# Kernel optimization log

Hardware: AMD Instinct MI355X
Metric: run time of the kernel (lower is better)

## Reference

```python
import jax, jax.numpy as jnp
import numpy as np

N = 20000      # total nodes (20 proteins x 1000 residues)
E = 320000     # edges (avg degree 16)
F_IN = 22      # amino-acid feature dim
H = 4          # attention heads
C = 64         # hidden dim per head
HC = H * C     # 256
G = 20         # number of graphs
OUT = 128      # output embedding dim
NEG_SLOPE = 0.2


def setup_inputs() -> dict:
    key = jax.random.key(0)
    ks = jax.random.split(key, 24)
    x = jax.random.normal(ks[0], (N, F_IN), dtype=jnp.float32)
    edge_index = jax.random.randint(ks[1], (2, E), 0, N)
    batch = jnp.arange(N, dtype=jnp.int64) // (N // G)  # 1000 nodes per graph
    s = 0.1
    d = {
        'x': x, 'edge_index': edge_index, 'batch': batch,
        'Win': jax.random.normal(ks[2], (F_IN, C)) * s,
        'bin_': jnp.zeros((C,), jnp.float32),
        'Wout': jax.random.normal(ks[3], (2 * HC, OUT)) * s,
        'bout': jnp.zeros((OUT,), jnp.float32),
    }
    kidx = 4
    for i in range(3):
        in_dim = C if i == 0 else HC
        d[f'Wl{i}'] = jax.random.normal(ks[kidx], (in_dim, HC)) * s; kidx += 1
        d[f'Wr{i}'] = jax.random.normal(ks[kidx], (in_dim, HC)) * s; kidx += 1
        d[f'att{i}'] = jax.random.normal(ks[kidx], (H, C)) * s; kidx += 1
        d[f'b{i}'] = jnp.zeros((HC,), jnp.float32)
    return d


def _gatv2_layer(h, src, dst, Wl, Wr, att, bias):
    # PyG GATv2Conv (share_weights=False, concat=True), dropout off (eval)
    xl = (h @ Wl).reshape(-1, H, C)   # source transform (x_j)
    xr = (h @ Wr).reshape(-1, H, C)   # target transform (x_i)
    e = jax.nn.leaky_relu(xl[src] + xr[dst], NEG_SLOPE)  # [E+N, H, C]
    logit = jnp.einsum('ehc,hc->eh', e, att)             # [E+N, H]
    mx = jax.ops.segment_max(logit, dst, num_segments=N)
    mx = jnp.where(jnp.isfinite(mx), mx, 0.0)
    ex = jnp.exp(logit - mx[dst])
    den = jax.ops.segment_sum(ex, dst, num_segments=N)
    alpha = ex / (den[dst] + 1e-16)                      # segment softmax
    out = jax.ops.segment_sum(alpha[:, :, None] * xl[src], dst, num_segments=N)
    return out.reshape(-1, HC) + bias


def reference(x, edge_index, batch, Win, bin_,
              Wl0, Wr0, att0, b0, Wl1, Wr1, att1, b1, Wl2, Wr2, att2, b2,
              Wout, bout):
    # add self-loops once (add_self_loops=True in every GATv2Conv)
    loops = jnp.arange(N, dtype=edge_index.dtype)
    src = jnp.concatenate([edge_index[0], loops])
    dst = jnp.concatenate([edge_index[1], loops])

    h = jax.nn.relu(x @ Win + bin_)  # input_proj + ReLU (dropout = eval identity)
    layers = [(Wl0, Wr0, att0, b0), (Wl1, Wr1, att1, b1), (Wl2, Wr2, att2, b2)]
    for (Wl, Wr, att, b) in layers:
        h_prev = h
        h = jax.nn.elu(_gatv2_layer(h, src, dst, Wl, Wr, att, b))
        if h_prev.shape[-1] == h.shape[-1]:  # residual when dims match (layers 1,2)
            h = h + h_prev

    counts = jax.ops.segment_sum(jnp.ones((N,), h.dtype), batch, num_segments=G)
    x_mean = jax.ops.segment_sum(h, batch, num_segments=G) / counts[:, None]
    x_max = jax.ops.segment_max(h, batch, num_segments=G)
    x_global = jnp.concatenate([x_mean, x_max], axis=-1)  # [G, 512]
    return x_global @ Wout + bout                          # [G, 128]
```

## Files before the change

kernel.cpp:

```cpp
#include <hip/hip_runtime.h>
#include <hip/hip_bf16.h>
#include <math.h>

#define N_NODES 20000
#define N_EDGES 320000
#define F_IN 22
#define H_HEADS 4
#define C_DIM 64
#define HC 256
#define G_GRAPHS 20
#define OUT_DIM 128
#define NODES_PER_G 1000
#define POOL_CHUNKS 8
#define NODES_PER_CHUNK (NODES_PER_G / POOL_CHUNKS)
#define ELL_CAP 64
#define SCAT_NB ((N_EDGES + 255) / 256)
#define INPROJ_NB (N_NODES / 4)
#define GAT_NB (N_NODES / 4)
#define GAT_CPX (GAT_NB / 8)

#if __has_builtin(__builtin_amdgcn_exp2f)
#define EXP2F __builtin_amdgcn_exp2f
#else
#define EXP2F exp2f
#endif

typedef unsigned short ushortT;
typedef __attribute__((ext_vector_type(8))) short short8;
typedef __attribute__((ext_vector_type(4))) float v4f;
typedef __attribute__((ext_vector_type(2))) float f2;

typedef const __attribute__((address_space(1))) void* gas_p;
typedef __attribute__((address_space(3))) void* las_p;

__device__ inline ushortT f2bf(float f) {
    unsigned int u = __float_as_uint(f);
    unsigned int r = (u + 0x7fffu + ((u >> 16) & 1u)) >> 16;
    return (ushortT)r;
}

__global__ __launch_bounds__(256) void front_kernel(
        const int* __restrict__ esrc, const int* __restrict__ edst,
        int* __restrict__ fill, int* __restrict__ ell,
        const float* __restrict__ x, const float* __restrict__ Win,
        const float* __restrict__ bin, ushortT* __restrict__ h0b,
        const float* __restrict__ Wl0, const float* __restrict__ Wr0,
        const float* __restrict__ Wl1, const float* __restrict__ Wr1,
        const float* __restrict__ Wl2, const float* __restrict__ Wr2,
        ushortT* __restrict__ Bt0, ushortT* __restrict__ Bt1, ushortT* __restrict__ Bt2) {
    int tid = threadIdx.x;
    if (blockIdx.x < SCAT_NB) {
        int i = blockIdx.x * 256 + tid;
        if (i < N_EDGES) {
            int d = edst[i];
            int p = atomicAdd(&fill[d], 1);
            if (p < ELL_CAP) ell[(d << 6) + p] = esrc[i];
        }
        return;
    }
    if (blockIdx.x < SCAT_NB + INPROJ_NB) {
        int node = (blockIdx.x - SCAT_NB) * 4 + (tid >> 6);
        int c = tid & 63;
        float acc = bin[c];
        const float* xr = x + node * F_IN;
#pragma unroll
        for (int f = 0; f < F_IN; f++) acc += xr[f] * Win[f * C_DIM + c];
        h0b[node * C_DIM + c] = f2bf(acc > 0.f ? acc : 0.f);
        return;
    }
    int flat = blockIdx.x - SCAT_NB - INPROJ_NB;
    int z = flat >> 6;
    int rem = flat & 63;
    int kx = (rem >> 3) * 32;
    int nx = (rem & 7) * 32;
    int layer = z >> 1, isR = z & 1;
    const float* src; ushortT* dst; int K;
    if (layer == 0)      { K = 64;  dst = Bt0; src = isR ? Wr0 : Wl0; }
    else if (layer == 1) { K = 256; dst = Bt1; src = isR ? Wr1 : Wl1; }
    else                 { K = 256; dst = Bt2; src = isR ? Wr2 : Wl2; }
    if (kx >= K) return;
    __shared__ float tile[32][33];
    int c = tid & 31, r8 = tid >> 5;
#pragma unroll
    for (int i = 0; i < 4; i++) {
        int kk = r8 + i * 8;
        tile[kk][c] = src[(kx + kk) * 256 + nx + c];
    }
    __syncthreads();
    int nbase = isR ? 256 : 0;
#pragma unroll
    for (int i = 0; i < 4; i++) {
        int nn = r8 + i * 8;
        dst[(size_t)(nbase + nx + nn) * K + kx + c] = f2bf(tile[c][nn]);
    }
}

#define GBM 128
#define GBN 128
#define GBK 32

__global__ __launch_bounds__(256) void gemm_mfma_kernel(
        const ushortT* __restrict__ A, const ushortT* __restrict__ Bt,
        ushortT* __restrict__ XLb, ushortT* __restrict__ XRb, int M, int K) {
    __shared__ ushortT As[GBM * GBK];
    __shared__ ushortT Bs[GBN * GBK];
    int tid = threadIdx.x;
    int wave = tid >> 6, lane = tid & 63;
    int wm = wave & 1, wn = wave >> 1;
    int bm0 = blockIdx.y * GBM;
    int bn0 = blockIdx.x * GBN;

    v4f acc[4][4];
#pragma unroll
    for (int mt = 0; mt < 4; mt++)
#pragma unroll
        for (int nt = 0; nt < 4; nt++) acc[mt][nt] = (v4f){0.f, 0.f, 0.f, 0.f};

    int srow = lane >> 2;
    int scol = (lane & 3) * 8;
    int arow0 = wave * 16 + srow;
    int arow1 = arow0 + 64;
    int ag0 = bm0 + arow0; if (ag0 >= M) ag0 = 0;
    int ag1 = bm0 + arow1; if (ag1 >= M) ag1 = 0;
    const ushortT* aptr0 = A + (size_t)ag0 * K + scol;
    const ushortT* aptr1 = A + (size_t)ag1 * K + scol;
    const ushortT* bptr0 = Bt + (size_t)(bn0 + arow0) * K + scol;
    const ushortT* bptr1 = Bt + (size_t)(bn0 + arow1) * K + scol;
    las_p lA0 = (las_p)&As[(wave * 16) * GBK];
    las_p lA1 = (las_p)&As[(wave * 16 + 64) * GBK];
    las_p lB0 = (las_p)&Bs[(wave * 16) * GBK];
    las_p lB1 = (las_p)&Bs[(wave * 16 + 64) * GBK];

    int mrow = lane & 15;
    int koff = (lane >> 4) * 8;

    for (int k0 = 0; k0 < K; k0 += GBK) {
        __builtin_amdgcn_global_load_lds((gas_p)(aptr0 + k0), lA0, 16, 0, 0);
        __builtin_amdgcn_global_load_lds((gas_p)(aptr1 + k0), lA1, 16, 0, 0);
        __builtin_amdgcn_global_load_lds((gas_p)(bptr0 + k0), lB0, 16, 0, 0);
        __builtin_amdgcn_global_load_lds((gas_p)(bptr1 + k0), lB1, 16, 0, 0);
        __syncthreads();
        short8 af[4], bf[4];
#pragma unroll
        for (int mt = 0; mt < 4; mt++)
            af[mt] = *(const short8*)&As[(wm * 64 + mt * 16 + mrow) * GBK + koff];
#pragma unroll
        for (int nt = 0; nt < 4; nt++)
            bf[nt] = *(const short8*)&Bs[(wn * 64 + nt * 16 + mrow) * GBK + koff];
#pragma unroll
        for (int mt = 0; mt < 4; mt++)
#pragma unroll
            for (int nt = 0; nt < 4; nt++)
                acc[mt][nt] = __builtin_amdgcn_mfma_f32_16x16x32_bf16(af[mt], bf[nt], acc[mt][nt], 0, 0, 0);
        __syncthreads();
    }

    int cbase = bn0 + wn * 64;
    ushortT* dst = XLb;
    if (cbase >= 256) { dst = XRb; cbase -= 256; }
    int col = cbase + (lane & 15);
    int rbase = bm0 + wm * 64 + ((lane >> 4) * 4);
#pragma unroll
    for (int mt = 0; mt < 4; mt++) {
#pragma unroll
        for (int reg = 0; reg < 4; reg++) {
            int row = rbase + mt * 16 + reg;
            if (row < M) {
#pragma unroll
                for (int nt = 0; nt < 4; nt++)
                    dst[(size_t)row * 256 + col + nt * 16] = f2bf(acc[mt][nt][reg]);
            }
        }
    }
}

template <int PAT>
__device__ inline float swz_add(float p) {
    return p + __int_as_float(__builtin_amdgcn_ds_swizzle(__float_as_int(p), PAT));
}

__device__ inline void gat_edge(uint2 curu, f2 xr01, f2 xr23, f2 at01, f2 at23,
                                float live, float& den, f2& acc01, f2& acc23) {
    f2 x01, x23;
    x01.x = __uint_as_float(curu.x << 16);
    x01.y = __uint_as_float(curu.x & 0xffff0000u);
    x23.x = __uint_as_float(curu.y << 16);
    x23.y = __uint_as_float(curu.y & 0xffff0000u);
    f2 t01 = x01 + xr01;
    f2 t23 = x23 + xr23;
    t01 = __builtin_elementwise_max(t01, t01 * 0.2f);
    t23 = __builtin_elementwise_max(t23, t23 * 0.2f);
    f2 pp = t01 * at01;
    pp = __builtin_elementwise_fma(t23, at23, pp);
    float p = pp.x + pp.y;
    p = swz_add<0x041F>(p);
    p = swz_add<0x081F>(p);
    p = swz_add<0x101F>(p);
    p = swz_add<0x201F>(p);
    p = fminf(p, 110.f);
    float w = EXP2F(p) * live;
    den += w;
    f2 wv = {w, w};
    acc01 = __builtin_elementwise_fma(wv, x01, acc01);
    acc23 = __builtin_elementwise_fma(wv, x23, acc23);
}

__global__ __launch_bounds__(256) void gat_layer_kernel(
        const ushortT* __restrict__ xlb, const ushortT* __restrict__ xrb,
        const int* __restrict__ ell, const int* __restrict__ fill,
        const float* __restrict__ att, const float* __restrict__ bias,
        const float* __restrict__ hprev,
        float* __restrict__ hout, ushortT* __restrict__ houtb) {
    int lane = threadIdx.x & 63;
    int bid = blockIdx.x;
    int lb = (bid & 7) * GAT_CPX + (bid >> 3);
    int d = lb * 4 + (threadIdx.x >> 6);

    const uint2* xl2 = (const uint2*)xlb;
    uint2 xru = ((const uint2*)xrb)[d * 64 + lane];
    f2 xr01, xr23;
    xr01.x = __uint_as_float(xru.x << 16);
    xr01.y = __uint_as_float(xru.x & 0xffff0000u);
    xr23.x = __uint_as_float(xru.y << 16);
    xr23.y = __uint_as_float(xru.y & 0xffff0000u);

    float4 attv = ((const float4*)att)[lane];
    const float LOG2E = 1.44269504088896f;
    f2 at01 = {attv.x * LOG2E, attv.y * LOG2E};
    f2 at23 = {attv.z * LOG2E, attv.w * LOG2E};

    int deg = fill[d];
    if (deg > ELL_CAP - 1) deg = ELL_CAP - 1;
    int M = deg + 1;

    int idx = (lane < deg) ? ell[(d << 6) + lane] : d;

    float den = 0.f;
    f2 acc01 = {0.f, 0.f}, acc23 = {0.f, 0.f};

    uint2 buf[4];
#pragma unroll
    for (int k = 0; k < 4; k++) {
        int ni = __builtin_amdgcn_readlane(idx, k);
        buf[k] = xl2[(size_t)ni * 64 + lane];
    }
    int P = (M + 3) >> 2;
    for (int g = 0; g < P; g++) {
        int base = g * 4;
#pragma unroll
        for (int k = 0; k < 4; k++) {
            uint2 cur = buf[k];
            int ni = __builtin_amdgcn_readlane(idx, (base + 4 + k) & 63);
            buf[k] = xl2[(size_t)ni * 64 + lane];
            float live = (base + k < M) ? 1.0f : 0.0f;
            gat_edge(cur, xr01, xr23, at01, at23, live, den, acc01, acc23);
        }
    }

    float inv = 1.f / (den + 1e-16f);
    float4 bv = ((const float4*)bias)[lane];
    float4 v;
    v.x = acc01.x * inv + bv.x;
    v.y = acc01.y * inv + bv.y;
    v.z = acc23.x * inv + bv.z;
    v.w = acc23.y * inv + bv.w;
    v.x = v.x > 0.f ? v.x : __expf(v.x) - 1.f;
    v.y = v.y > 0.f ? v.y : __expf(v.y) - 1.f;
    v.z = v.z > 0.f ? v.z : __expf(v.z) - 1.f;
    v.w = v.w > 0.f ? v.w : __expf(v.w) - 1.f;
    if (hprev) {
        float4 hp = ((const float4*)hprev)[d * 64 + lane];
        v.x += hp.x; v.y += hp.y; v.z += hp.z; v.w += hp.w;
    }
    if (hout) ((float4*)hout)[d * 64 + lane] = v;
    uint2 pb;
    pb.x = (unsigned int)f2bf(v.x) | ((unsigned int)f2bf(v.y) << 16);
    pb.y = (unsigned int)f2bf(v.z) | ((unsigned int)f2bf(v.w) << 16);
    ((uint2*)houtb)[d * 64 + lane] = pb;
}

__global__ __launch_bounds__(256) void pool_partial_kernel(
        const ushortT* __restrict__ hb, float* __restrict__ psum, float* __restrict__ pmax) {
    int blk = blockIdx.x;
    int tid = threadIdx.x;
    int g = blk / POOL_CHUNKS;
    int ch = blk % POOL_CHUNKS;
    const ushortT* base = hb + ((size_t)g * NODES_PER_G + ch * NODES_PER_CHUNK) * HC;
    float sum = 0.f, mx = -INFINITY;
    for (int n = 0; n < NODES_PER_CHUNK; n++) {
        float v = __uint_as_float(((unsigned int)base[n * HC + tid]) << 16);
        sum += v;
        mx = fmaxf(mx, v);
    }
    psum[blk * HC + tid] = sum;
    pmax[blk * HC + tid] = mx;
}

__global__ __launch_bounds__(256) void pool_out_kernel(
        const float* __restrict__ psum, const float* __restrict__ pmax,
        const float* __restrict__ Wout, const float* __restrict__ bout,
        float* __restrict__ out) {
    int g = blockIdx.x;
    int tid = threadIdx.x;
    __shared__ float xg[2 * HC];
    float sum = 0.f, mx = -INFINITY;
    for (int c = 0; c < POOL_CHUNKS; c++) {
        sum += psum[(g * POOL_CHUNKS + c) * HC + tid];
        mx = fmaxf(mx, pmax[(g * POOL_CHUNKS + c) * HC + tid]);
    }
    xg[tid] = sum * (1.0f / NODES_PER_G);
    xg[HC + tid] = mx;
    __syncthreads();
    if (tid < OUT_DIM) {
        float acc = bout[tid];
        for (int j = 0; j < 2 * HC; j++) acc += xg[j] * Wout[j * OUT_DIM + tid];
        out[g * OUT_DIM + tid] = acc;
    }
}


extern "C" void kernel_launch(void* const* d_in, const int* in_sizes, int n_in,
                              void* d_out, int out_size, void* d_ws, size_t ws_size,
                              hipStream_t stream) {
    const float* x    = (const float*)d_in[0];
    const int*   ei   = (const int*)d_in[1];
    const float* Win  = (const float*)d_in[3];
    const float* bin  = (const float*)d_in[4];
    const float* Wout = (const float*)d_in[5];
    const float* bout = (const float*)d_in[6];
    const float* Wl[3] = {(const float*)d_in[7],  (const float*)d_in[11], (const float*)d_in[15]};
    const float* Wr[3] = {(const float*)d_in[8],  (const float*)d_in[12], (const float*)d_in[16]};
    const float* att[3] = {(const float*)d_in[9], (const float*)d_in[13], (const float*)d_in[17]};
    const float* bb[3] = {(const float*)d_in[10], (const float*)d_in[14], (const float*)d_in[18]};
    float* out = (float*)d_out;

    const int* esrc = ei;
    const int* edst = ei + N_EDGES;

    float* hA   = (float*)d_ws;
    float* hB   = hA + (size_t)N_NODES * HC;
    float* psum = hB + (size_t)N_NODES * HC;
    float* pmax = psum + (size_t)G_GRAPHS * POOL_CHUNKS * HC;
    ushortT* h0b = (ushortT*)(pmax + (size_t)G_GRAPHS * POOL_CHUNKS * HC);
    ushortT* hAb = h0b + (size_t)N_NODES * C_DIM;
    ushortT* hBb = hAb + (size_t)N_NODES * HC;
    ushortT* XLb = hBb + (size_t)N_NODES * HC;
    ushortT* XRb = XLb + (size_t)N_NODES * HC;
    ushortT* Bt0 = XRb + (size_t)N_NODES * HC;
    ushortT* Bt1 = Bt0 + 512 * 64;
    ushortT* Bt2 = Bt1 + 512 * 256;
    int* fill  = (int*)(Bt2 + 512 * 256);
    int* ell   = fill + N_NODES;

    (void)hipMemsetAsync(fill, 0, N_NODES * sizeof(int), stream);

    front_kernel<<<SCAT_NB + INPROJ_NB + 384, 256, 0, stream>>>(
        esrc, edst, fill, ell, x, Win, bin, h0b,
        Wl[0], Wr[0], Wl[1], Wr[1], Wl[2], Wr[2], Bt0, Bt1, Bt2);

    dim3 ggrid(512 / GBN, (N_NODES + GBM - 1) / GBM);

    gemm_mfma_kernel<<<ggrid, 256, 0, stream>>>(h0b, Bt0, XLb, XRb, N_NODES, C_DIM);
    gat_layer_kernel<<<GAT_NB, 256, 0, stream>>>(XLb, XRb, ell, fill, att[0], bb[0],
                                                 nullptr, hA, hAb);

    gemm_mfma_kernel<<<ggrid, 256, 0, stream>>>(hAb, Bt1, XLb, XRb, N_NODES, HC);
    gat_layer_kernel<<<GAT_NB, 256, 0, stream>>>(XLb, XRb, ell, fill, att[1], bb[1],
                                                 hA, hB, hBb);

    gemm_mfma_kernel<<<ggrid, 256, 0, stream>>>(hBb, Bt2, XLb, XRb, N_NODES, HC);
    gat_layer_kernel<<<GAT_NB, 256, 0, stream>>>(XLb, XRb, ell, fill, att[2], bb[2],
                                                 hB, nullptr, hAb);

    pool_partial_kernel<<<G_GRAPHS * POOL_CHUNKS, 256, 0, stream>>>(hAb, psum, pmax);
    pool_out_kernel<<<G_GRAPHS, 256, 0, stream>>>(psum, pmax, Wout, bout, out);
}
```

Baseline: 263.1 us.

## Process two edges per wavefront with 16-byte loads per lane in GAT layer

Splits each 64-lane wavefront into two 32-lane halves. Each half handles a different neighbor edge and each lane loads 8 bf16 features as a uint4 instead of 4. The head-dot reduction drops one swizzle step, and the halves' partial softmax sums and accumulators are combined with a cross-half shuffle at the end. This aims to halve loop iterations and widen the gather loads, at the cost of more registers, a final reduction, and idle lanes in the store phase.

Measured after the change: 263.3 us. Within noise of the previous version (+0.1%).

```diff
diff --git a/kernel.cpp b/kernel.cpp
--- a/kernel.cpp
+++ b/kernel.cpp
@@ -179,30 +179,44 @@
     return p + __int_as_float(__builtin_amdgcn_ds_swizzle(__float_as_int(p), PAT));
 }
 
-__device__ inline void gat_edge(uint2 curu, f2 xr01, f2 xr23, f2 at01, f2 at23,
-                                float live, float& den, f2& acc01, f2& acc23) {
-    f2 x01, x23;
+__device__ inline void gat_edge2(uint4 curu,
+        f2 xr01, f2 xr23, f2 xr45, f2 xr67,
+        f2 a01, f2 a23, f2 a45, f2 a67,
+        float live, float& den,
+        f2& acc01, f2& acc23, f2& acc45, f2& acc67) {
+    f2 x01, x23, x45, x67;
     x01.x = __uint_as_float(curu.x << 16);
     x01.y = __uint_as_float(curu.x & 0xffff0000u);
     x23.x = __uint_as_float(curu.y << 16);
     x23.y = __uint_as_float(curu.y & 0xffff0000u);
+    x45.x = __uint_as_float(curu.z << 16);
+    x45.y = __uint_as_float(curu.z & 0xffff0000u);
+    x67.x = __uint_as_float(curu.w << 16);
+    x67.y = __uint_as_float(curu.w & 0xffff0000u);
     f2 t01 = x01 + xr01;
     f2 t23 = x23 + xr23;
+    f2 t45 = x45 + xr45;
+    f2 t67 = x67 + xr67;
     t01 = __builtin_elementwise_max(t01, t01 * 0.2f);
     t23 = __builtin_elementwise_max(t23, t23 * 0.2f);
-    f2 pp = t01 * at01;
-    pp = __builtin_elementwise_fma(t23, at23, pp);
+    t45 = __builtin_elementwise_max(t45, t45 * 0.2f);
+    t67 = __builtin_elementwise_max(t67, t67 * 0.2f);
+    f2 pp = t01 * a01;
+    pp = __builtin_elementwise_fma(t23, a23, pp);
+    pp = __builtin_elementwise_fma(t45, a45, pp);
+    pp = __builtin_elementwise_fma(t67, a67, pp);
     float p = pp.x + pp.y;
     p = swz_add<0x041F>(p);
     p = swz_add<0x081F>(p);
     p = swz_add<0x101F>(p);
-    p = swz_add<0x201F>(p);
     p = fminf(p, 110.f);
     float w = EXP2F(p) * live;
     den += w;
     f2 wv = {w, w};
     acc01 = __builtin_elementwise_fma(wv, x01, acc01);
     acc23 = __builtin_elementwise_fma(wv, x23, acc23);
+    acc45 = __builtin_elementwise_fma(wv, x45, acc45);
+    acc67 = __builtin_elementwise_fma(wv, x67, acc67);
 }
 
 __global__ __launch_bounds__(256) void gat_layer_kernel(
@@ -212,22 +226,32 @@
         const float* __restrict__ hprev,
         float* __restrict__ hout, ushortT* __restrict__ houtb) {
     int lane = threadIdx.x & 63;
+    int q = lane & 31;
+    int half = lane >> 5;
     int bid = blockIdx.x;
     int lb = (bid & 7) * GAT_CPX + (bid >> 3);
     int d = lb * 4 + (threadIdx.x >> 6);
 
-    const uint2* xl2 = (const uint2*)xlb;
-    uint2 xru = ((const uint2*)xrb)[d * 64 + lane];
-    f2 xr01, xr23;
+    const uint4* xl4 = (const uint4*)xlb;
+    uint4 xru = ((const uint4*)xrb)[d * 32 + q];
+    f2 xr01, xr23, xr45, xr67;
     xr01.x = __uint_as_float(xru.x << 16);
     xr01.y = __uint_as_float(xru.x & 0xffff0000u);
     xr23.x = __uint_as_float(xru.y << 16);
     xr23.y = __uint_as_float(xru.y & 0xffff0000u);
-
-    float4 attv = ((const float4*)att)[lane];
+    xr45.x = __uint_as_float(xru.z << 16);
+    xr45.y = __uint_as_float(xru.z & 0xffff0000u);
+    xr67.x = __uint_as_float(xru.w << 16);
+    xr67.y = __uint_as_float(xru.w & 0xffff0000u);
+
+    const float4* att4 = (const float4*)att;
+    float4 av0 = att4[q * 2];
+    float4 av1 = att4[q * 2 + 1];
     const float LOG2E = 1.44269504088896f;
-    f2 at01 = {attv.x * LOG2E, attv.y * LOG2E};
-    f2 at23 = {attv.z * LOG2E, attv.w * LOG2E};
+    f2 a01 = {av0.x * LOG2E, av0.y * LOG2E};
+    f2 a23 = {av0.z * LOG2E, av0.w * LOG2E};
+    f2 a45 = {av1.x * LOG2E, av1.y * LOG2E};
+    f2 a67 = {av1.z * LOG2E, av1.w * LOG2E};
 
     int deg = fill[d];
     if (deg > ELL_CAP - 1) deg = ELL_CAP - 1;
@@ -236,47 +260,81 @@
     int idx = (lane < deg) ? ell[(d << 6) + lane] : d;
 
     float den = 0.f;
-    f2 acc01 = {0.f, 0.f}, acc23 = {0.f, 0.f};
-
-    uint2 buf[4];
-#pragma unroll
-    for (int k = 0; k < 4; k++) {
-        int ni = __builtin_amdgcn_readlane(idx, k);
-        buf[k] = xl2[(size_t)ni * 64 + lane];
-    }
-    int P = (M + 3) >> 2;
-    for (int g = 0; g < P; g++) {
-        int base = g * 4;
-#pragma unroll
-        for (int k = 0; k < 4; k++) {
-            uint2 cur = buf[k];
-            int ni = __builtin_amdgcn_readlane(idx, (base + 4 + k) & 63);
-            buf[k] = xl2[(size_t)ni * 64 + lane];
-            float live = (base + k < M) ? 1.0f : 0.0f;
-            gat_edge(cur, xr01, xr23, at01, at23, live, den, acc01, acc23);
+    f2 acc01 = {0.f, 0.f}, acc23 = {0.f, 0.f}, acc45 = {0.f, 0.f}, acc67 = {0.f, 0.f};
+
+    uint4 buf[2];
+#pragma unroll
+    for (int k = 0; k < 2; k++) {
+        int sA = __builtin_amdgcn_readlane(idx, 2 * k);
+        int sB = __builtin_amdgcn_readlane(idx, 2 * k + 1);
+        int ni = half ? sB : sA;
+        buf[k] = xl4[(size_t)ni * 32 + q];
+    }
+    int P2 = (M + 1) >> 1;
+    int G = (P2 + 1) >> 1;
+    for (int g = 0; g < G; g++) {
+#pragma unroll
+        for (int k = 0; k < 2; k++) {
+            uint4 cur = buf[k];
+            int np = 2 * g + 2 + k;
+            int sA = __builtin_amdgcn_readlane(idx, (2 * np) & 63);
+            int sB = __builtin_amdgcn_readlane(idx, (2 * np + 1) & 63);
+            int ni = half ? sB : sA;
+            buf[k] = xl4[(size_t)ni * 32 + q];
+            int slot = (2 * g + k) * 2 + half;
+            float live = (slot < M) ? 1.0f : 0.0f;
+            gat_edge2(cur, xr01, xr23, xr45, xr67, a01, a23, a45, a67,
+                      live, den, acc01, acc23, acc45, acc67);
         }
     }
 
+    den     += __shfl_xor(den, 32);
+    acc01.x += __shfl_xor(acc01.x, 32);
+    acc01.y += __shfl_xor(acc01.y, 32);
+    acc23.x += __shfl_xor(acc23.x, 32);
+    acc23.y += __shfl_xor(acc23.y, 32);
+    acc45.x += __shfl_xor(acc45.x, 32);
+    acc45.y += __shfl_xor(acc45.y, 32);
+    acc67.x += __shfl_xor(acc67.x, 32);
+    acc67.y += __shfl_xor(acc67.y, 32);
+
     float inv = 1.f / (den + 1e-16f);
-    float4 bv = ((const float4*)bias)[lane];
-    float4 v;
-    v.x = acc01.x * inv + bv.x;
-    v.y = acc01.y * inv + bv.y;
-    v.z = acc23.x * inv + bv.z;
-    v.w = acc23.y * inv + bv.w;
-    v.x = v.x > 0.f ? v.x : __expf(v.x) - 1.f;
-    v.y = v.y > 0.f ? v.y : __expf(v.y) - 1.f;
-    v.z = v.z > 0.f ? v.z : __expf(v.z) - 1.f;
-    v.w = v.w > 0.f ? v.w : __expf(v.w) - 1.f;
+    float4 bv0 = ((const float4*)bias)[q * 2];
+    float4 bv1 = ((const float4*)bias)[q * 2 + 1];
+    float v0 = acc01.x * inv + bv0.x;
+    float v1 = acc01.y * inv + bv0.y;
+    float v2 = acc23.x * inv + bv0.z;
+    float v3 = acc23.y * inv + bv0.w;
+    float v4 = acc45.x * inv + bv1.x;
+    float v5 = acc45.y * inv + bv1.y;
+    float v6 = acc67.x * inv + bv1.z;
+    float v7 = acc67.y * inv + bv1.w;
+    v0 = v0 > 0.f ? v0 : __expf(v0) - 1.f;
+    v1 = v1 > 0.f ? v1 : __expf(v1) - 1.f;
+    v2 = v2 > 0.f ? v2 : __expf(v2) - 1.f;
+    v3 = v3 > 0.f ? v3 : __expf(v3) - 1.f;
+    v4 = v4 > 0.f ? v4 : __expf(v4) - 1.f;
+    v5 = v5 > 0.f ? v5 : __expf(v5) - 1.f;
+    v6 = v6 > 0.f ? v6 : __expf(v6) - 1.f;
+    v7 = v7 > 0.f ? v7 : __expf(v7) - 1.f;
     if (hprev) {
-        float4 hp = ((const float4*)hprev)[d * 64 + lane];
-        v.x += hp.x; v.y += hp.y; v.z += hp.z; v.w += hp.w;
-    }
-    if (hout) ((float4*)hout)[d * 64 + lane] = v;
-    uint2 pb;
-    pb.x = (unsigned int)f2bf(v.x) | ((unsigned int)f2bf(v.y) << 16);
-    pb.y = (unsigned int)f2bf(v.z) | ((unsigned int)f2bf(v.w) << 16);
-    ((uint2*)houtb)[d * 64 + lane] = pb;
+        float4 h0 = ((const float4*)hprev)[d * 64 + q * 2];
+        float4 h1 = ((const float4*)hprev)[d * 64 + q * 2 + 1];
+        v0 += h0.x; v1 += h0.y; v2 += h0.z; v3 += h0.w;
+        v4 += h1.x; v5 += h1.y; v6 += h1.z; v7 += h1.w;
+    }
+    if (half == 0) {
+        if (hout) {
+            ((float4*)hout)[d * 64 + q * 2]     = (float4){v0, v1, v2, v3};
+            ((float4*)hout)[d * 64 + q * 2 + 1] = (float4){v4, v5, v6, v7};
+        }
+        uint4 pb;
+        pb.x = (unsigned int)f2bf(v0) | ((unsigned int)f2bf(v1) << 16);
+        pb.y = (unsigned int)f2bf(v2) | ((unsigned int)f2bf(v3) << 16);
+        pb.z = (unsigned int)f2bf(v4) | ((unsigned int)f2bf(v5) << 16);
+        pb.w = (unsigned int)f2bf(v6) | ((unsigned int)f2bf(v7) << 16);
+        ((uint4*)houtb)[d * 32 + q] = pb;
+    }
 }
 
 __global__ __launch_bounds__(256) void pool_partial_kernel(
```

## Fuse all stages into one persistent cooperative kernel with grid syncs

Applied to the files above, without the earlier changes.

Replaces the sequence of separate kernel launches (front, three GEMM+GAT pairs, pooling) with a single cooperative persistent kernel that loops over work tiles and separates phases with grid-wide barriers. It also turns the weight-transpose tiles into plain grid-stride loops and raises the pooling chunk count. The aim is to remove the launch overhead and inter-kernel gaps. In exchange, occupancy is capped by the cooperative grid size, grid.sync adds its own cost, and the GAT phase loses its earlier block-to-node remapping. The weight transpose now uses uncoalesced strided reads.

Result: slower. 845.3 us (+221.2%).

```diff
diff --git a/kernel.cpp b/kernel.cpp
--- a/kernel.cpp
+++ b/kernel.cpp
@@ -1,6 +1,9 @@
 #include <hip/hip_runtime.h>
+#include <hip/hip_cooperative_groups.h>
 #include <hip/hip_bf16.h>
 #include <math.h>
+
+namespace cg = cooperative_groups;
 
 #define N_NODES 20000
 #define N_EDGES 320000
@@ -11,13 +14,10 @@
 #define G_GRAPHS 20
 #define OUT_DIM 128
 #define NODES_PER_G 1000
-#define POOL_CHUNKS 8
+#define POOL_CHUNKS 50
 #define NODES_PER_CHUNK (NODES_PER_G / POOL_CHUNKS)
 #define ELL_CAP 64
-#define SCAT_NB ((N_EDGES + 255) / 256)
-#define INPROJ_NB (N_NODES / 4)
 #define GAT_NB (N_NODES / 4)
-#define GAT_CPX (GAT_NB / 8)
 
 #if __has_builtin(__builtin_amdgcn_exp2f)
 #define EXP2F __builtin_amdgcn_exp2f
@@ -38,137 +38,88 @@
     unsigned int r = (u + 0x7fffu + ((u >> 16) & 1u)) >> 16;
     return (ushortT)r;
 }
-
-__global__ __launch_bounds__(256) void front_kernel(
-        const int* __restrict__ esrc, const int* __restrict__ edst,
-        int* __restrict__ fill, int* __restrict__ ell,
-        const float* __restrict__ x, const float* __restrict__ Win,
-        const float* __restrict__ bin, ushortT* __restrict__ h0b,
-        const float* __restrict__ Wl0, const float* __restrict__ Wr0,
-        const float* __restrict__ Wl1, const float* __restrict__ Wr1,
-        const float* __restrict__ Wl2, const float* __restrict__ Wr2,
-        ushortT* __restrict__ Bt0, ushortT* __restrict__ Bt1, ushortT* __restrict__ Bt2) {
-    int tid = threadIdx.x;
-    if (blockIdx.x < SCAT_NB) {
-        int i = blockIdx.x * 256 + tid;
-        if (i < N_EDGES) {
-            int d = edst[i];
-            int p = atomicAdd(&fill[d], 1);
-            if (p < ELL_CAP) ell[(d << 6) + p] = esrc[i];
-        }
-        return;
-    }
-    if (blockIdx.x < SCAT_NB + INPROJ_NB) {
-        int node = (blockIdx.x - SCAT_NB) * 4 + (tid >> 6);
-        int c = tid & 63;
-        float acc = bin[c];
-        const float* xr = x + node * F_IN;
-#pragma unroll
-        for (int f = 0; f < F_IN; f++) acc += xr[f] * Win[f * C_DIM + c];
-        h0b[node * C_DIM + c] = f2bf(acc > 0.f ? acc : 0.f);
-        return;
-    }
-    int flat = blockIdx.x - SCAT_NB - INPROJ_NB;
-    int z = flat >> 6;
-    int rem = flat & 63;
-    int kx = (rem >> 3) * 32;
-    int nx = (rem & 7) * 32;
-    int layer = z >> 1, isR = z & 1;
-    const float* src; ushortT* dst; int K;
-    if (layer == 0)      { K = 64;  dst = Bt0; src = isR ? Wr0 : Wl0; }
-    else if (layer == 1) { K = 256; dst = Bt1; src = isR ? Wr1 : Wl1; }
-    else                 { K = 256; dst = Bt2; src = isR ? Wr2 : Wl2; }
-    if (kx >= K) return;
-    __shared__ float tile[32][33];
-    int c = tid & 31, r8 = tid >> 5;
-#pragma unroll
-    for (int i = 0; i < 4; i++) {
-        int kk = r8 + i * 8;
-        tile[kk][c] = src[(kx + kk) * 256 + nx + c];
-    }
-    __syncthreads();
-    int nbase = isR ? 256 : 0;
-#pragma unroll
-    for (int i = 0; i < 4; i++) {
-        int nn = r8 + i * 8;
-        dst[(size_t)(nbase + nx + nn) * K + kx + c] = f2bf(tile[c][nn]);
-    }
+__device__ inline float bf2f(ushortT u) {
+    return __uint_as_float(((unsigned int)u) << 16);
 }
 
 #define GBM 128
 #define GBN 128
 #define GBK 32
 
-__global__ __launch_bounds__(256) void gemm_mfma_kernel(
-        const ushortT* __restrict__ A, const ushortT* __restrict__ Bt,
-        ushortT* __restrict__ XLb, ushortT* __restrict__ XRb, int M, int K) {
-    __shared__ ushortT As[GBM * GBK];
-    __shared__ ushortT Bs[GBN * GBK];
+__device__ inline void gemm_phase(const ushortT* __restrict__ A,
+                                  const ushortT* __restrict__ Bt,
+                                  ushortT* __restrict__ XLb, ushortT* __restrict__ XRb,
+                                  int K, ushortT* As, ushortT* Bs) {
+    const int M = N_NODES;
+    const int MT = (N_NODES + GBM - 1) / GBM;
     int tid = threadIdx.x;
     int wave = tid >> 6, lane = tid & 63;
     int wm = wave & 1, wn = wave >> 1;
-    int bm0 = blockIdx.y * GBM;
-    int bn0 = blockIdx.x * GBN;
-
-    v4f acc[4][4];
-#pragma unroll
-    for (int mt = 0; mt < 4; mt++)
-#pragma unroll
-        for (int nt = 0; nt < 4; nt++) acc[mt][nt] = (v4f){0.f, 0.f, 0.f, 0.f};
-
-    int srow = lane >> 2;
-    int scol = (lane & 3) * 8;
-    int arow0 = wave * 16 + srow;
-    int arow1 = arow0 + 64;
-    int ag0 = bm0 + arow0; if (ag0 >= M) ag0 = 0;
-    int ag1 = bm0 + arow1; if (ag1 >= M) ag1 = 0;
-    const ushortT* aptr0 = A + (size_t)ag0 * K + scol;
-    const ushortT* aptr1 = A + (size_t)ag1 * K + scol;
-    const ushortT* bptr0 = Bt + (size_t)(bn0 + arow0) * K + scol;
-    const ushortT* bptr1 = Bt + (size_t)(bn0 + arow1) * K + scol;
-    las_p lA0 = (las_p)&As[(wave * 16) * GBK];
-    las_p lA1 = (las_p)&As[(wave * 16 + 64) * GBK];
-    las_p lB0 = (las_p)&Bs[(wave * 16) * GBK];
-    las_p lB1 = (las_p)&Bs[(wave * 16 + 64) * GBK];
-
-    int mrow = lane & 15;
-    int koff = (lane >> 4) * 8;
-
-    for (int k0 = 0; k0 < K; k0 += GBK) {
-        __builtin_amdgcn_global_load_lds((gas_p)(aptr0 + k0), lA0, 16, 0, 0);
-        __builtin_amdgcn_global_load_lds((gas_p)(aptr1 + k0), lA1, 16, 0, 0);
-        __builtin_amdgcn_global_load_lds((gas_p)(bptr0 + k0), lB0, 16, 0, 0);
-        __builtin_amdgcn_global_load_lds((gas_p)(bptr1 + k0), lB1, 16, 0, 0);
-        __syncthreads();
-        short8 af[4], bf[4];
+
+    for (int t = blockIdx.x; t < MT * 4; t += gridDim.x) {
+        int bm0 = (t >> 2) * GBM;
+        int bn0 = (t & 3) * GBN;
+
+        v4f acc[4][4];
 #pragma unroll
         for (int mt = 0; mt < 4; mt++)
-            af[mt] = *(const short8*)&As[(wm * 64 + mt * 16 + mrow) * GBK + koff];
-#pragma unroll
-        for (int nt = 0; nt < 4; nt++)
-            bf[nt] = *(const short8*)&Bs[(wn * 64 + nt * 16 + mrow) * GBK + koff];
-#pragma unroll
-        for (int mt = 0; mt < 4; mt++)
+#pragma unroll
+            for (int nt = 0; nt < 4; nt++) acc[mt][nt] = (v4f){0.f, 0.f, 0.f, 0.f};
+
+        int srow = lane >> 2;
+        int scol = (lane & 3) * 8;
+        int arow0 = wave * 16 + srow;
+        int arow1 = arow0 + 64;
+        int ag0 = bm0 + arow0; if (ag0 >= M) ag0 = 0;
+        int ag1 = bm0 + arow1; if (ag1 >= M) ag1 = 0;
+        const ushortT* aptr0 = A + (size_t)ag0 * K + scol;
+        const ushortT* aptr1 = A + (size_t)ag1 * K + scol;
+        const ushortT* bptr0 = Bt + (size_t)(bn0 + arow0) * K + scol;
+        const ushortT* bptr1 = Bt + (size_t)(bn0 + arow1) * K + scol;
+        las_p lA0 = (las_p)&As[(wave * 16) * GBK];
+        las_p lA1 = (las_p)&As[(wave * 16 + 64) * GBK];
+        las_p lB0 = (las_p)&Bs[(wave * 16) * GBK];
+        las_p lB1 = (las_p)&Bs[(wave * 16 + 64) * GBK];
+
+        int mrow = lane & 15;
+        int koff = (lane >> 4) * 8;
+
+        for (int k0 = 0; k0 < K; k0 += GBK) {
+            __builtin_amdgcn_global_load_lds((gas_p)(aptr0 + k0), lA0, 16, 0, 0);
+            __builtin_amdgcn_global_load_lds((gas_p)(aptr1 + k0), lA1, 16, 0, 0);
+            __builtin_amdgcn_global_load_lds((gas_p)(bptr0 + k0), lB0, 16, 0, 0);
+            __builtin_amdgcn_global_load_lds((gas_p)(bptr1 + k0), lB1, 16, 0, 0);
+            __syncthreads();
+            short8 af[4], bf[4];
+#pragma unroll
+            for (int mt = 0; mt < 4; mt++)
+                af[mt] = *(const short8*)&As[(wm * 64 + mt * 16 + mrow) * GBK + koff];
 #pragma unroll
             for (int nt = 0; nt < 4; nt++)
-                acc[mt][nt] = __builtin_amdgcn_mfma_f32_16x16x32_bf16(af[mt], bf[nt], acc[mt][nt], 0, 0, 0);
-        __syncthreads();
-    }
-
-    int cbase = bn0 + wn * 64;
-    ushortT* dst = XLb;
-    if (cbase >= 256) { dst = XRb; cbase -= 256; }
-    int col = cbase + (lane & 15);
-    int rbase = bm0 + wm * 64 + ((lane >> 4) * 4);
-#pragma unroll
-    for (int mt = 0; mt < 4; mt++) {
-#pragma unroll
-        for (int reg = 0; reg < 4; reg++) {
-            int row = rbase + mt * 16 + reg;
-            if (row < M) {
+                bf[nt] = *(const short8*)&Bs[(wn * 64 + nt * 16 + mrow) * GBK + koff];
+#pragma unroll
+            for (int mt = 0; mt < 4; mt++)
 #pragma unroll
                 for (int nt = 0; nt < 4; nt++)
-                    dst[(size_t)row * 256 + col + nt * 16] = f2bf(acc[mt][nt][reg]);
+                    acc[mt][nt] = __builtin_amdgcn_mfma_f32_16x16x32_bf16(af[mt], bf[nt], acc[mt][nt], 0, 0, 0);
+            __syncthreads();
+        }
+
+        int cbase = bn0 + wn * 64;
+        ushortT* dst = XLb;
+        if (cbase >= 256) { dst = XRb; cbase -= 256; }
+        int col = cbase + (lane & 15);
+        int rbase = bm0 + wm * 64 + ((lane >> 4) * 4);
+#pragma unroll
+        for (int mt = 0; mt < 4; mt++) {
+#pragma unroll
+            for (int reg = 0; reg < 4; reg++) {
+                int row = rbase + mt * 16 + reg;
+                if (row < M) {
+#pragma unroll
+                    for (int nt = 0; nt < 4; nt++)
+                        dst[(size_t)row * 256 + col + nt * 16] = f2bf(acc[mt][nt][reg]);
+                }
             }
         }
     }
@@ -205,116 +156,178 @@
     acc23 = __builtin_elementwise_fma(wv, x23, acc23);
 }
 
-__global__ __launch_bounds__(256) void gat_layer_kernel(
-        const ushortT* __restrict__ xlb, const ushortT* __restrict__ xrb,
-        const int* __restrict__ ell, const int* __restrict__ fill,
-        const float* __restrict__ att, const float* __restrict__ bias,
-        const float* __restrict__ hprev,
-        float* __restrict__ hout, ushortT* __restrict__ houtb) {
+__device__ inline void gat_phase(const ushortT* __restrict__ xlb, const ushortT* __restrict__ xrb,
+                                 const int* __restrict__ ell, const int* __restrict__ fill,
+                                 const float* __restrict__ att, const float* __restrict__ bias,
+                                 const float* __restrict__ hprev,
+                                 float* __restrict__ hout, ushortT* __restrict__ houtb) {
     int lane = threadIdx.x & 63;
+    const uint2* xl2 = (const uint2*)xlb;
+
+    for (int lb = blockIdx.x; lb < GAT_NB; lb += gridDim.x) {
+        int d = lb * 4 + (threadIdx.x >> 6);
+
+        uint2 xru = ((const uint2*)xrb)[d * 64 + lane];
+        f2 xr01, xr23;
+        xr01.x = __uint_as_float(xru.x << 16);
+        xr01.y = __uint_as_float(xru.x & 0xffff0000u);
+        xr23.x = __uint_as_float(xru.y << 16);
+        xr23.y = __uint_as_float(xru.y & 0xffff0000u);
+
+        float4 attv = ((const float4*)att)[lane];
+        const float LOG2E = 1.44269504088896f;
+        f2 at01 = {attv.x * LOG2E, attv.y * LOG2E};
+        f2 at23 = {attv.z * LOG2E, attv.w * LOG2E};
+
+        int deg = fill[d];
+        if (deg > ELL_CAP - 1) deg = ELL_CAP - 1;
+        int M = deg + 1;
+
+        int idx = (lane < deg) ? ell[(d << 6) + lane] : d;
+
+        float den = 0.f;
+        f2 acc01 = {0.f, 0.f}, acc23 = {0.f, 0.f};
+
+        uint2 buf[4];
+#pragma unroll
+        for (int k = 0; k < 4; k++) {
+            int ni = __builtin_amdgcn_readlane(idx, k);
+            buf[k] = xl2[(size_t)ni * 64 + lane];
+        }
+        int P = (M + 3) >> 2;
+        for (int g = 0; g < P; g++) {
+            int base = g * 4;
+#pragma unroll
+            for (int k = 0; k < 4; k++) {
+                uint2 cur = buf[k];
+                int ni = __builtin_amdgcn_readlane(idx, (base + 4 + k) & 63);
+                buf[k] = xl2[(size_t)ni * 64 + lane];
+                float live = (base + k < M) ? 1.0f : 0.0f;
+                gat_edge(cur, xr01, xr23, at01, at23, live, den, acc01, acc23);
+            }
+        }
+
+        float inv = 1.f / (den + 1e-16f);
+        float4 bv = ((const float4*)bias)[lane];
+        float4 v;
+        v.x = acc01.x * inv + bv.x;
+        v.y = acc01.y * inv + bv.y;
+        v.z = acc23.x * inv + bv.z;
+        v.w = acc23.y * inv + bv.w;
+        v.x = v.x > 0.f ? v.x : __expf(v.x) - 1.f;
+        v.y = v.y > 0.f ? v.y : __expf(v.y) - 1.f;
+        v.z = v.z > 0.f ? v.z : __expf(v.z) - 1.f;
+        v.w = v.w > 0.f ? v.w : __expf(v.w) - 1.f;
+        if (hprev) {
+            float4 hp = ((const float4*)hprev)[d * 64 + lane];
+            v.x += hp.x; v.y += hp.y; v.z += hp.z; v.w += hp.w;
+        }
+        if (hout) ((float4*)hout)[d * 64 + lane] = v;
+        uint2 pb;
+        pb.x = (unsigned int)f2bf(v.x) | ((unsigned int)f2bf(v.y) << 16);
+        pb.y = (unsigned int)f2bf(v.z) | ((unsigned int)f2bf(v.w) << 16);
+        ((uint2*)houtb)[d * 64 + lane] = pb;
+    }
+}
+
+struct MegaParams {
+    const int *esrc, *edst;
+    int *fill, *ell;
+    const float *x, *Win, *bin;
+    ushortT *h0b;
+    const float *Wl0, *Wr0, *Wl1, *Wr1, *Wl2, *Wr2;
+    ushortT *Bt0, *Bt1, *Bt2;
+    ushortT *XLb, *XRb;
+    const float *att0, *b0, *att1, *b1, *att2, *b2;
+    float *hA, *hB;
+    ushortT *hAb, *hBb;
+    float *psum, *pmax;
+    const float *Wout, *bout;
+    float *out;
+};
+
+__global__ __launch_bounds__(256, 4) void mega_kernel(MegaParams p) {
+    cg::grid_group grid = cg::this_grid();
+    __shared__ __align__(16) unsigned char smem[GBM * GBK * 2 * sizeof(ushortT)];
+    ushortT* As = (ushortT*)smem;
+    ushortT* Bs = As + GBM * GBK;
+
+    int tid = threadIdx.x;
     int bid = blockIdx.x;
-    int lb = (bid & 7) * GAT_CPX + (bid >> 3);
-    int d = lb * 4 + (threadIdx.x >> 6);
-
-    const uint2* xl2 = (const uint2*)xlb;
-    uint2 xru = ((const uint2*)xrb)[d * 64 + lane];
-    f2 xr01, xr23;
-    xr01.x = __uint_as_float(xru.x << 16);
-    xr01.y = __uint_as_float(xru.x & 0xffff0000u);
-    xr23.x = __uint_as_float(xru.y << 16);
-    xr23.y = __uint_as_float(xru.y & 0xffff0000u);
-
-    float4 attv = ((const float4*)att)[lane];
-    const float LOG2E = 1.44269504088896f;
-    f2 at01 = {attv.x * LOG2E, attv.y * LOG2E};
-    f2 at23 = {attv.z * LOG2E, attv.w * LOG2E};
-
-    int deg = fill[d];
-    if (deg > ELL_CAP - 1) deg = ELL_CAP - 1;
-    int M = deg + 1;
-
-    int idx = (lane < deg) ? ell[(d << 6) + lane] : d;
-
-    float den = 0.f;
-    f2 acc01 = {0.f, 0.f}, acc23 = {0.f, 0.f};
-
-    uint2 buf[4];
-#pragma unroll
-    for (int k = 0; k < 4; k++) {
-        int ni = __builtin_amdgcn_readlane(idx, k);
-        buf[k] = xl2[(size_t)ni * 64 + lane];
-    }
-    int P = (M + 3) >> 2;
-    for (int g = 0; g < P; g++) {
-        int base = g * 4;
-#pragma unroll
-        for (int k = 0; k < 4; k++) {
-            uint2 cur = buf[k];
-            int ni = __builtin_amdgcn_readlane(idx, (base + 4 + k) & 63);
-            buf[k] = xl2[(size_t)ni * 64 + lane];
-            float live = (base + k < M) ? 1.0f : 0.0f;
-            gat_edge(cur, xr01, xr23, at01, at23, live, den, acc01, acc23);
-        }
-    }
-
-    float inv = 1.f / (den + 1e-16f);
-    float4 bv = ((const float4*)bias)[lane];
-    float4 v;
-    v.x = acc01.x * inv + bv.x;
-    v.y = acc01.y * inv + bv.y;
-    v.z = acc23.x * inv + bv.z;
-    v.w = acc23.y * inv + bv.w;
-    v.x = v.x > 0.f ? v.x : __expf(v.x) - 1.f;
-    v.y = v.y > 0.f ? v.y : __expf(v.y) - 1.f;
-    v.z = v.z > 0.f ? v.z : __expf(v.z) - 1.f;
-    v.w = v.w > 0.f ? v.w : __expf(v.w) - 1.f;
-    if (hprev) {
-        float4 hp = ((const float4*)hprev)[d * 64 + lane];
-        v.x += hp.x; v.y += hp.y; v.z += hp.z; v.w += hp.w;
-    }
-    if (hout) ((float4*)hout)[d * 64 + lane] = v;
-    uint2 pb;
-    pb.x = (unsigned int)f2bf(v.x) | ((unsigned int)f2bf(v.y) << 16);
-    pb.y = (unsigned int)f2bf(v.z) | ((unsigned int)f2bf(v.w) << 16);
-    ((uint2*)houtb)[d * 64 + lane] = pb;
-}
-
-__global__ __launch_bounds__(256) void pool_partial_kernel(
-        const ushortT* __restrict__ hb, float* __restrict__ psum, float* __restrict__ pmax) {
-    int blk = blockIdx.x;
-    int tid = threadIdx.x;
-    int g = blk / POOL_CHUNKS;
-    int ch = blk % POOL_CHUNKS;
-    const ushortT* base = hb + ((size_t)g * NODES_PER_G + ch * NODES_PER_CHUNK) * HC;
-    float sum = 0.f, mx = -INFINITY;
-    for (int n = 0; n < NODES_PER_CHUNK; n++) {
-        float v = __uint_as_float(((unsigned int)base[n * HC + tid]) << 16);
-        sum += v;
-        mx = fmaxf(mx, v);
-    }
-    psum[blk * HC + tid] = sum;
-    pmax[blk * HC + tid] = mx;
-}
-
-__global__ __launch_bounds__(256) void pool_out_kernel(
-        const float* __restrict__ psum, const float* __restrict__ pmax,
-        const float* __restrict__ Wout, const float* __restrict__ bout,
-        float* __restrict__ out) {
-    int g = blockIdx.x;
-    int tid = threadIdx.x;
-    __shared__ float xg[2 * HC];
-    float sum = 0.f, mx = -INFINITY;
-    for (int c = 0; c < POOL_CHUNKS; c++) {
-        sum += psum[(g * POOL_CHUNKS + c) * HC + tid];
-        mx = fmaxf(mx, pmax[(g * POOL_CHUNKS + c) * HC + tid]);
-    }
-    xg[tid] = sum * (1.0f / NODES_PER_G);
-    xg[HC + tid] = mx;
-    __syncthreads();
-    if (tid < OUT_DIM) {
-        float acc = bout[tid];
-        for (int j = 0; j < 2 * HC; j++) acc += xg[j] * Wout[j * OUT_DIM + tid];
-        out[g * OUT_DIM + tid] = acc;
+    int nthr = gridDim.x * 256;
+    int gtid = bid * 256 + tid;
+
+    for (int i = gtid; i < N_EDGES; i += nthr) {
+        int d = p.edst[i];
+        int s = atomicAdd(&p.fill[d], 1);
+        if (s < ELL_CAP) p.ell[(d << 6) + s] = p.esrc[i];
+    }
+    for (int w = gtid; w < N_NODES * C_DIM; w += nthr) {
+        int node = w >> 6, c = w & 63;
+        float acc = p.bin[c];
+        const float* xr = p.x + node * F_IN;
+#pragma unroll
+        for (int f = 0; f < F_IN; f++) acc += xr[f] * p.Win[f * C_DIM + c];
+        p.h0b[w] = f2bf(acc > 0.f ? acc : 0.f);
+    }
+    for (int w = gtid; w < 512 * C_DIM; w += nthr) {
+        int n = w >> 6, k = w & 63;
+        const float* W = (n < 256) ? p.Wl0 : p.Wr0;
+        p.Bt0[w] = f2bf(W[k * 256 + (n & 255)]);
+    }
+    for (int w = gtid; w < 512 * 256; w += nthr) {
+        int n = w >> 8, k = w & 255;
+        const float* W1 = (n < 256) ? p.Wl1 : p.Wr1;
+        const float* W2 = (n < 256) ? p.Wl2 : p.Wr2;
+        p.Bt1[w] = f2bf(W1[k * 256 + (n & 255)]);
+        p.Bt2[w] = f2bf(W2[k * 256 + (n & 255)]);
+    }
+    grid.sync();
+
+    gemm_phase(p.h0b, p.Bt0, p.XLb, p.XRb, C_DIM, As, Bs);
+    grid.sync();
+    gat_phase(p.XLb, p.XRb, p.ell, p.fill, p.att0, p.b0, nullptr, p.hA, p.hAb);
+    grid.sync();
+    gemm_phase(p.hAb, p.Bt1, p.XLb, p.XRb, HC, As, Bs);
+    grid.sync();
+    gat_phase(p.XLb, p.XRb, p.ell, p.fill, p.att1, p.b1, p.hA, p.hB, p.hBb);
+    grid.sync();
+    gemm_phase(p.hBb, p.Bt2, p.XLb, p.XRb, HC, As, Bs);
+    grid.sync();
+    gat_phase(p.XLb, p.XRb, p.ell, p.fill, p.att2, p.b2, p.hB, nullptr, p.hAb);
+    grid.sync();
+
+    for (int blk = bid; blk < G_GRAPHS * POOL_CHUNKS; blk += gridDim.x) {
+        int g = blk / POOL_CHUNKS;
+        int ch = blk % POOL_CHUNKS;
+        const ushortT* base = p.hAb + ((size_t)g * NODES_PER_G + ch * NODES_PER_CHUNK) * HC;
+        float sum = 0.f, mx = -INFINITY;
+        for (int n = 0; n < NODES_PER_CHUNK; n++) {
+            float v = bf2f(base[n * HC + tid]);
+            sum += v;
+            mx = fmaxf(mx, v);
+        }
+        p.psum[blk * HC + tid] = sum;
+        p.pmax[blk * HC + tid] = mx;
+    }
+    grid.sync();
+
+    for (int g = bid; g < G_GRAPHS; g += gridDim.x) {
+        float* xg = (float*)smem;
+        float sum = 0.f, mx = -INFINITY;
+        for (int c = 0; c < POOL_CHUNKS; c++) {
+            sum += p.psum[(g * POOL_CHUNKS + c) * HC + tid];
+            mx = fmaxf(mx, p.pmax[(g * POOL_CHUNKS + c) * HC + tid]);
+        }
+        xg[tid] = sum * (1.0f / NODES_PER_G);
+        xg[HC + tid] = mx;
+        __syncthreads();
+        if (tid < OUT_DIM) {
+            float acc = p.bout[tid];
+            for (int j = 0; j < 2 * HC; j++) acc += xg[j] * p.Wout[j * OUT_DIM + tid];
+            p.out[g * OUT_DIM + tid] = acc;
+        }
+        __syncthreads();
     }
 }
 
@@ -354,24 +367,27 @@
 
     (void)hipMemsetAsync(fill, 0, N_NODES * sizeof(int), stream);
 
-    front_kernel<<<SCAT_NB + INPROJ_NB + 384, 256, 0, stream>>>(
-        esrc, edst, fill, ell, x, Win, bin, h0b,
-        Wl[0], Wr[0], Wl[1], Wr[1], Wl[2], Wr[2], Bt0, Bt1, Bt2);
-
-    dim3 ggrid(512 / GBN, (N_NODES + GBM - 1) / GBM);
-
-    gemm_mfma_kernel<<<ggrid, 256, 0, stream>>>(h0b, Bt0, XLb, XRb, N_NODES, C_DIM);
-    gat_layer_kernel<<<GAT_NB, 256, 0, stream>>>(XLb, XRb, ell, fill, att[0], bb[0],
-                                                 nullptr, hA, hAb);
-
-    gemm_mfma_kernel<<<ggrid, 256, 0, stream>>>(hAb, Bt1, XLb, XRb, N_NODES, HC);
-    gat_layer_kernel<<<GAT_NB, 256, 0, stream>>>(XLb, XRb, ell, fill, att[1], bb[1],
-                                                 hA, hB, hBb);
-
-    gemm_mfma_kernel<<<ggrid, 256, 0, stream>>>(hBb, Bt2, XLb, XRb, N_NODES, HC);
-    gat_layer_kernel<<<GAT_NB, 256, 0, stream>>>(XLb, XRb, ell, fill, att[2], bb[2],
-                                                 hB, nullptr, hAb);
-
-    pool_partial_kernel<<<G_GRAPHS * POOL_CHUNKS, 256, 0, stream>>>(hAb, psum, pmax);
-    pool_out_kernel<<<G_GRAPHS, 256, 0, stream>>>(psum, pmax, Wout, bout, out);
-}
+    static int coopGrid = 0;
+    if (coopGrid == 0) {
+        int mb = 0;
+        if (hipOccupancyMaxActiveBlocksPerMultiprocessor(&mb, mega_kernel, 256, 0) != hipSuccess || mb < 1)
+            mb = 1;
+        if (mb > 4) mb = 4;
+        coopGrid = mb * 256;
+    }
+
+    MegaParams p;
+    p.esrc = esrc; p.edst = edst; p.fill = fill; p.ell = ell;
+    p.x = x; p.Win = Win; p.bin = bin; p.h0b = h0b;
+    p.Wl0 = Wl[0]; p.Wr0 = Wr[0]; p.Wl1 = Wl[1]; p.Wr1 = Wr[1]; p.Wl2 = Wl[2]; p.Wr2 = Wr[2];
+    p.Bt0 = Bt0; p.Bt1 = Bt1; p.Bt2 = Bt2;
+    p.XLb = XLb; p.XRb = XRb;
+    p.att0 = att[0]; p.b0 = bb[0]; p.att1 = att[1]; p.b1 = bb[1]; p.att2 = att[2]; p.b2 = bb[2];
+    p.hA = hA; p.hB = hB; p.hAb = hAb; p.hBb = hBb;
+    p.psum = psum; p.pmax = pmax;
+    p.Wout = Wout; p.bout = bout; p.out = out;
+
+    void* args[] = {&p};
+    (void)hipLaunchCooperativeKernel((const void*)mega_kernel, dim3(coopGrid), dim3(256),
+                                     args, 0, stream);
+}
```
